# Kernel optimization log

Measured on AMD Instinct MI355X. Metric: run time of the kernel, lower is better.

Reference implementation:

```python
import jax, jax.numpy as jnp
import numpy as np

N = 50000   # nodes
E = 800000  # edges (avg degree 16)
G = 64      # graphs in batch
H = 4       # attention heads
D = 128     # hidden dim per head (= hidden_dim)
V = 128     # embedding vocab (input_dim)
NEG_SLOPE = 0.2

def setup_inputs() -> dict:
    key = jax.random.key(0)
    ks = jax.random.split(key, 12)
    s = 0.05
    return {
        "feats": jax.random.randint(ks[0], (N,), 0, V),
        "src": jax.random.randint(ks[1], (E,), 0, N),
        "dst": jax.random.randint(ks[2], (E,), 0, N),
        "graph_ids": jnp.sort(jax.random.randint(ks[3], (N,), 0, G)),
        "emb": jax.random.normal(ks[4], (V, D)) * s,
        "W1": jax.random.normal(ks[5], (D, H * D)) * s,
        "b1": jax.random.normal(ks[6], (H * D,)) * s,
        "a1": jax.random.normal(ks[7], (H, D)) * s,
        "W2": jax.random.normal(ks[8], (D, H * D)) * s,
        "b2": jax.random.normal(ks[9], (H * D,)) * s,
        "a2": jax.random.normal(ks[10], (H, D)) * s,
        "Wreg": jax.random.normal(ks[11], (1, D)) * s,
    }

def gatv2_layer(x, W, b, a, src, dst):
    # shared-weight GATv2: h = Wx + b, split into heads -> [N,H,D]
    h = (x @ W + b).reshape(-1, H, D)
    hs = h[src]                      # [E,H,D] source feats per edge
    hd = h[dst]                      # [E,H,D] dest feats per edge
    e = jax.nn.leaky_relu(hs + hd, NEG_SLOPE)
    logits = jnp.einsum('ehd,hd->eh', e, a)          # [E,H]
    # edge softmax over incoming edges of each dst node
    m = jax.ops.segment_max(logits, dst, num_segments=N)
    m = jnp.where(jnp.isfinite(m), m, 0.0)           # empty segments -> 0 (unused)
    ex = jnp.exp(logits - m[dst])
    denom = jax.ops.segment_sum(ex, dst, num_segments=N)
    alpha = ex / denom[dst]                          # [E,H]
    rst = jax.ops.segment_sum(alpha[:, :, None] * hs, dst, num_segments=N)  # [N,H,D]
    return rst.mean(axis=1)          # .mean(dim=1) over heads -> [N,D]

def reference(feats, src, dst, graph_ids, emb, W1, b1, a1, W2, b2, a2, Wreg):
    x = emb[feats]                                   # embedding lookup [N,D]
    x = gatv2_layer(x, W1, b1, a1, src, dst)         # layer 1 (dropout=0)
    x = gatv2_layer(x, W2, b2, a2, src, dst)         # layer 2
    pooled = jax.ops.segment_sum(x, graph_ids, num_segments=G)  # SumPooling [G,D]
    return pooled @ Wreg.T                           # Linear bias=False -> [G,1]
```

## Files before the change

kernel.cpp:

```cpp
#include <hip/hip_runtime.h>
#include <hip/hip_bf16.h>

#define N_NODES 50000
#define N_EDGES 800000
#define G_GRAPHS 64
#define H_HEADS 4
#define D_DIM 128
#define HD 512
#define V_VOCAB 128
#define NEG_SLOPE 0.2f

typedef float f32x2v __attribute__((ext_vector_type(2)));
typedef float f32x4 __attribute__((ext_vector_type(4)));
typedef short s16x8 __attribute__((ext_vector_type(8)));
typedef _Float16 h16x2 __attribute__((ext_vector_type(2)));

static __device__ __forceinline__ unsigned short f2b(float f) {
    union { float f; unsigned int i; } x; x.f = f;
    unsigned int r = x.i + 0x7fffu + ((x.i >> 16) & 1u);
    return (unsigned short)(r >> 16);
}
static __device__ __forceinline__ h16x2 u2h2(unsigned int u) {
    union { unsigned int u; h16x2 h; } c; c.u = u; return c.h;
}
static __device__ __forceinline__ unsigned int h22u(h16x2 h) {
    union { unsigned int u; h16x2 h; } c; c.h = h; return c.u;
}
static __device__ __forceinline__ h16x2 packf2(float lo, float hi) {
    union { __fp16 __attribute__((ext_vector_type(2))) p; h16x2 h; } c;
    c.p = __builtin_amdgcn_cvt_pkrtz(lo, hi);
    return c.h;
}

#if __has_builtin(__builtin_amdgcn_cvt_scalef32_pk_f16_fp8)
static __device__ __forceinline__ void fp8x4_to_h16(unsigned int u, h16x2& h0, h16x2& h1) {
    auto r0 = __builtin_amdgcn_cvt_scalef32_pk_f16_fp8((int)u, 1.0f, false);
    auto r1 = __builtin_amdgcn_cvt_scalef32_pk_f16_fp8((int)u, 1.0f, true);
    union { decltype(r0) p; h16x2 h; } c0, c1;
    c0.p = r0; c1.p = r1;
    h0 = c0.h; h1 = c1.h;
}
#else
static __device__ __forceinline__ void fp8x4_to_h16(unsigned int u, h16x2& h0, h16x2& h1) {
    f32x2v lo = __builtin_amdgcn_cvt_pk_f32_fp8(u, false);
    f32x2v hi = __builtin_amdgcn_cvt_pk_f32_fp8(u, true);
    h0 = packf2(lo.x, lo.y);
    h1 = packf2(hi.x, hi.y);
}
#endif

template<int CTRL>
static __device__ __forceinline__ float dpp_add(float v) {
    union { float f; int i; } a, b;
    a.f = v;
    b.i = __builtin_amdgcn_mov_dpp(a.i, CTRL, 0xF, 0xF, true);
    return v + b.f;
}
static __device__ __forceinline__ float row16_sum(float p) {
    p = dpp_add<0xB1>(p);
    p = dpp_add<0x4E>(p);
    p = dpp_add<0x141>(p);
    p = dpp_add<0x140>(p);
    return p;
}

#define MEGA_M1_BLOCKS   64
#define MEGA_WSZ_BLOCKS  256
#define MEGA_HIST_BLOCKS ((N_EDGES + 255) / 256)
__global__ void __launch_bounds__(256) mega_kernel(const float* __restrict__ emb,
                                                   const float* __restrict__ W1,
                                                   const float* __restrict__ b1,
                                                   unsigned int* __restrict__ M1b,
                                                   const float* __restrict__ W2,
                                                   unsigned short* __restrict__ Wb,
                                                   const int* __restrict__ dst,
                                                   int* __restrict__ counts,
                                                   float* __restrict__ pool) {
    int b = blockIdx.x;
    if (b < MEGA_M1_BLOCKS) {
        int idx = b * 256 + threadIdx.x;
        int v = idx >> 7, c0 = (idx & 127) * 4;
        float acc[4] = {b1[c0], b1[c0 + 1], b1[c0 + 2], b1[c0 + 3]};
        for (int k = 0; k < 128; k++) {
            float e = emb[v * 128 + k];
            #pragma unroll
            for (int j = 0; j < 4; j++) acc[j] = fmaf(e, W1[k * 512 + c0 + j], acc[j]);
        }
        unsigned int pk = __builtin_amdgcn_cvt_pk_fp8_f32(acc[0], acc[1], 0, false);
        pk = __builtin_amdgcn_cvt_pk_fp8_f32(acc[2], acc[3], pk, true);
        M1b[idx] = pk;
    } else if (b < MEGA_M1_BLOCKS + MEGA_WSZ_BLOCKS) {
        int idx = (b - MEGA_M1_BLOCKS) * 256 + threadIdx.x;
        int j = idx & 7, c = (idx >> 3) & 511, qq = idx >> 12;
        Wb[idx] = f2b(W2[(qq * 8 + j) * 512 + c]);
    } else {
        int hb = b - MEGA_M1_BLOCKS - MEGA_WSZ_BLOCKS;
        if (hb == 0 && threadIdx.x < G_GRAPHS) pool[threadIdx.x] = 0.f;
        int i = hb * 256 + threadIdx.x;
        if (i < N_EDGES) atomicAdd(&counts[dst[i]], 1);
    }
}

__global__ void __launch_bounds__(256) scanf_kernel(const int* __restrict__ counts,
                                                    int* __restrict__ offsets,
                                                    int* __restrict__ cursor,
                                                    int* __restrict__ bsum,
                                                    int* __restrict__ flag) {
    __shared__ int buf[256];
    __shared__ int sbase;
    int t = threadIdx.x, b = blockIdx.x;
    int i0 = (b * 256 + t) * 4;
    int v[4], c[4], s = 0;
    #pragma unroll
    for (int j = 0; j < 4; j++) {
        int idx = i0 + j;
        v[j] = (idx < N_NODES) ? counts[idx] : 0;
        s += v[j];
        c[j] = s;
    }
    buf[t] = s;
    __syncthreads();
    for (int off = 1; off < 256; off <<= 1) {
        int add = (t >= off) ? buf[t - off] : 0;
        __syncthreads();
        buf[t] += add;
        __syncthreads();
    }
    int ebase = (t > 0) ? buf[t - 1] : 0;
    if (t == 0) {
        bsum[b] = buf[255];
        __threadfence();
        atomicAdd(flag, 1);
        while (atomicAdd(flag, 0) < 64) __builtin_amdgcn_s_sleep(8);
    }
    __syncthreads();
    if (t < 64) {
        int vv = (t < b) ? atomicAdd(&bsum[t], 0) : 0;
        #pragma unroll
        for (int off = 1; off < 64; off <<= 1) vv += __shfl_xor(vv, off);
        if (t == 0) sbase = vv;
    }
    __syncthreads();
    int base = sbase;
    #pragma unroll
    for (int j = 0; j < 4; j++) {
        int idx = i0 + j;
        if (idx < N_NODES) {
            int e = base + ebase + c[j];
            offsets[idx + 1] = e;
            cursor[idx] = e - v[j];
        }
    }
    if (b == 0 && t == 0) offsets[0] = 0;
}

__global__ void scatter_kernel(const int* __restrict__ src, const int* __restrict__ dst,
                               int* __restrict__ cursor, int* __restrict__ csr_src) {
    int i = blockIdx.x * blockDim.x + threadIdx.x;
    if (i < N_EDGES) {
        int d = dst[i];
        int pos = atomicAdd(&cursor[d], 1);
        csr_src[pos] = src[i];
    }
}

template<bool LAYER1>
__global__ void __launch_bounds__(256) gat_kernel(const unsigned int* __restrict__ h,
                                                  const int* __restrict__ offsets,
                                                  const int* __restrict__ csr_src,
                                                  const int* __restrict__ feats,
                                                  const float* __restrict__ a,
                                                  const float* __restrict__ wreg,
                                                  unsigned short* __restrict__ x,
                                                  float* __restrict__ dots) {
    int wid = threadIdx.x >> 6;
    int lane = threadIdx.x & 63;
    int n = blockIdx.x * 4 + wid;
    if (n >= N_NODES) return;
    n = __builtin_amdgcn_readfirstlane(n);
    int row_s = __builtin_amdgcn_readfirstlane(offsets[n]);
    int row_e = __builtin_amdgcn_readfirstlane(offsets[n + 1]);
    int cnt = row_e - row_s;
    int voff = lane * 2;

    h16x2 hd2[4], a06[4], a04[4], acc2[4];
    float pd;
    {
        int nr = LAYER1 ? __builtin_amdgcn_readfirstlane(feats[n]) : n;
        uint2 hv = *reinterpret_cast<const uint2*>(&h[(unsigned)nr * 128u + voff]);
        fp8x4_to_h16(hv.x, hd2[0], hd2[1]);
        fp8x4_to_h16(hv.y, hd2[2], hd2[3]);
        float4 av0 = *reinterpret_cast<const float4*>(&a[lane * 8]);
        float4 av1 = *reinterpret_cast<const float4*>(&a[lane * 8 + 4]);
        float aa[8] = {av0.x, av0.y, av0.z, av0.w, av1.x, av1.y, av1.z, av1.w};
        const float L2E = 1.4426950408889634f;
        #pragma unroll
        for (int k = 0; k < 4; k++) {
            a06[k][0] = (_Float16)(aa[2*k]   * (0.6f * L2E));
            a06[k][1] = (_Float16)(aa[2*k+1] * (0.6f * L2E));
            a04[k][0] = (_Float16)(aa[2*k]   * (0.4f * L2E));
            a04[k][1] = (_Float16)(aa[2*k+1] * (0.4f * L2E));
            acc2[k][0] = (_Float16)0.f; acc2[k][1] = (_Float16)0.f;
        }
        float s = 0.f;
        #pragma unroll
        for (int k = 0; k < 4; k++) s = __builtin_amdgcn_fdot2(hd2[k], a06[k], s, false);
        pd = row16_sum(s);
    }

    auto ld = [&](int ii) {
        int s = __builtin_amdgcn_readfirstlane(csr_src[row_s + ii]);
        if (LAYER1) s = __builtin_amdgcn_readfirstlane(feats[s]);
        return *reinterpret_cast<const uint2*>(&h[(unsigned)s * 128u + voff]);
    };

    float den = 0.f;
    uint2 rA = make_uint2(0, 0), rB = make_uint2(0, 0);
    if (cnt > 0) rA = ld(0);
    if (cnt > 1) rB = ld(1);

    const float C1 = 0.69314718f, C2 = 0.24022651f, C3 = 0.05550411f;

    auto process = [&](uint2 sv) {
        h16x2 hs[4];
        fp8x4_to_h16(sv.x, hs[0], hs[1]);
        fp8x4_to_h16(sv.y, hs[2], hs[3]);
        float p0 = 0.f, p1 = 0.f;
        #pragma unroll
        for (int k = 0; k < 2; k++) {
            h16x2 t2 = hs[k] + hd2[k];
            h16x2 at2 = u2h2(h22u(t2) & 0x7FFF7FFFu);
            p0 = __builtin_amdgcn_fdot2(hs[k], a06[k], p0, false);
            p0 = __builtin_amdgcn_fdot2(at2, a04[k], p0, false);
        }
        #pragma unroll
        for (int k = 2; k < 4; k++) {
            h16x2 t2 = hs[k] + hd2[k];
            h16x2 at2 = u2h2(h22u(t2) & 0x7FFF7FFFu);
            p1 = __builtin_amdgcn_fdot2(hs[k], a06[k], p1, false);
            p1 = __builtin_amdgcn_fdot2(at2, a04[k], p1, false);
        }
        float p = row16_sum(p0 + p1) + pd;
        float w = fmaf(p, fmaf(p, fmaf(p, C3, C2), C1), 1.f);
        den += w;
        h16x2 w2 = packf2(w, w);
        #pragma unroll
        for (int k = 0; k < 4; k++) acc2[k] = w2 * hs[k] + acc2[k];
    };

    for (int i = 0; i < cnt; i += 2) {
        {
            uint2 cur = rA;
            rA = ld(min(i + 2, cnt - 1));
            process(cur);
        }
        if (i + 1 < cnt) {
            uint2 cur = rB;
            rB = ld(min(i + 3, cnt - 1));
            process(cur);
        }
    }

    float inv = (den > 0.f) ? 0.25f / den : 0.f;
    float out8[8];
    #pragma unroll
    for (int j = 0; j < 8; j++) {
        float r = (float)acc2[j >> 1][j & 1] * inv;
        r += __shfl_xor(r, 16);
        r += __shfl_xor(r, 32);
        out8[j] = r;
    }
    if constexpr (LAYER1) {
        if (lane < 16) {
            union { unsigned short u[8]; uint4 v; } o;
            #pragma unroll
            for (int j = 0; j < 8; j++) o.u[j] = f2b(out8[j]);
            *reinterpret_cast<uint4*>(&x[(unsigned)n * 128u + lane * 8]) = o.v;
        }
    } else {
        int d0 = (lane & 15) * 8;
        float4 wv0 = *reinterpret_cast<const float4*>(&wreg[d0]);
        float4 wv1 = *reinterpret_cast<const float4*>(&wreg[d0 + 4]);
        float pdot = out8[0] * wv0.x + out8[1] * wv0.y + out8[2] * wv0.z + out8[3] * wv0.w
                   + out8[4] * wv1.x + out8[5] * wv1.y + out8[6] * wv1.z + out8[7] * wv1.w;
        pdot = row16_sum(pdot);
        if (lane == 0) dots[n] = pdot;
    }
}

__global__ void __launch_bounds__(256) gemm_kernel(const unsigned short* __restrict__ x,
                                                   const unsigned short* __restrict__ Wb,
                                                   const float* __restrict__ bias,
                                                   unsigned char* __restrict__ hout) {
    int w = threadIdx.x >> 6, l = threadIdx.x & 63;
    int rb = blockIdx.y * 64 + w * 16;
    int cb = blockIdx.x * 64;
    int lr = l & 15, lq = l >> 4;
    f32x4 acc[4] = {};
    int arow = rb + lr;
    bool rok = arow < N_NODES;
    #pragma unroll
    for (int s = 0; s < 4; s++) {
        s16x8 afr = {};
        if (rok) afr = *reinterpret_cast<const s16x8*>(&x[(size_t)arow * 128 + s * 32 + lq * 8]);
        #pragma unroll
        for (int sub = 0; sub < 4; sub++) {
            s16x8 bfr = *reinterpret_cast<const s16x8*>(
                &Wb[(((size_t)(s * 4 + lq) * 512) + cb + sub * 16 + lr) << 3]);
            acc[sub] = __builtin_amdgcn_mfma_f32_16x16x32_bf16(bfr, afr, acc[sub], 0, 0, 0);
        }
    }
    if (!rok) return;
    #pragma unroll
    for (int sub = 0; sub < 4; sub++) {
        int col0 = cb + sub * 16 + lq * 4;
        float4 bb = *reinterpret_cast<const float4*>(&bias[col0]);
        unsigned int pk = __builtin_amdgcn_cvt_pk_fp8_f32(acc[sub][0] + bb.x,
                                                          acc[sub][1] + bb.y, 0, false);
        pk = __builtin_amdgcn_cvt_pk_fp8_f32(acc[sub][2] + bb.z,
                                             acc[sub][3] + bb.w, pk, true);
        *reinterpret_cast<unsigned int*>(&hout[(size_t)arow * 512 + col0]) = pk;
    }
}

__global__ void __launch_bounds__(256) pool64_kernel(const float* __restrict__ dots,
                                                     const int* __restrict__ gid,
                                                     float* __restrict__ pool,
                                                     int* __restrict__ done,
                                                     float* __restrict__ out) {
    int wave = (blockIdx.x * blockDim.x + threadIdx.x) >> 6;
    int lane = threadIdx.x & 63;
    int n0 = wave * 64;
    if (n0 < N_NODES) {
        int n = n0 + lane;
        int nc = min(n, N_NODES - 1);
        int g = gid[nc];
        float v = (n < N_NODES) ? dots[n] : 0.f;
        int g0 = __shfl(g, 0);
        bool uni = __all(g == g0);
        if (uni) {
            v += __shfl_xor(v, 1);
            v += __shfl_xor(v, 2);
            v += __shfl_xor(v, 4);
            v += __shfl_xor(v, 8);
            v += __shfl_xor(v, 16);
            v += __shfl_xor(v, 32);
            if (lane == 0) atomicAdd(&pool[g0], v);
        } else {
            if (n < N_NODES) atomicAdd(&pool[g], v);
        }
    }
    __threadfence();
    __syncthreads();
    __shared__ int amlast;
    if (threadIdx.x == 0)
        amlast = (atomicAdd(done, 1) == (int)gridDim.x - 1) ? 1 : 0;
    __syncthreads();
    if (amlast && threadIdx.x < G_GRAPHS) {
        out[threadIdx.x] = atomicAdd(&pool[threadIdx.x], 0.f);
    }
}

extern "C" void kernel_launch(void* const* d_in, const int* in_sizes, int n_in,
                              void* d_out, int out_size, void* d_ws, size_t ws_size,
                              hipStream_t stream) {
    const int* feats = (const int*)d_in[0];
    const int* src   = (const int*)d_in[1];
    const int* dst   = (const int*)d_in[2];
    const int* gids  = (const int*)d_in[3];
    const float* emb  = (const float*)d_in[4];
    const float* W1   = (const float*)d_in[5];
    const float* b1   = (const float*)d_in[6];
    const float* a1   = (const float*)d_in[7];
    const float* W2   = (const float*)d_in[8];
    const float* b2   = (const float*)d_in[9];
    const float* a2   = (const float*)d_in[10];
    const float* wreg = (const float*)d_in[11];
    float* out = (float*)d_out;

    char* ws = (char*)d_ws;
    size_t off = 0;
    auto alloc = [&](size_t bytes) -> void* {
        void* p = ws + off;
        off = (off + bytes + 255) & ~(size_t)255;
        return p;
    };
    int*   counts  = (int*)alloc((size_t)N_NODES * 4 + 8);
    int*   flag    = counts + N_NODES;
    int*   done    = counts + N_NODES + 1;
    int*   offsets = (int*)alloc((size_t)(N_NODES + 1) * 4);
    int*   cursor  = (int*)alloc((size_t)N_NODES * 4);
    int*   csr_src = (int*)alloc((size_t)N_EDGES * 4);
    int*   bsum    = (int*)alloc(64 * 4);
    unsigned int*   M1b = (unsigned int*)alloc((size_t)V_VOCAB * HD);
    unsigned int*   h  = (unsigned int*)alloc((size_t)N_NODES * HD);
    unsigned short* x  = (unsigned short*)alloc((size_t)N_NODES * D_DIM * 2);
    unsigned short* Wb = (unsigned short*)alloc((size_t)D_DIM * HD * 2);
    float* dots    = (float*)alloc((size_t)N_NODES * 4);
    float* pool    = (float*)alloc((size_t)G_GRAPHS * 4);

    hipMemsetAsync(counts, 0, (size_t)N_NODES * 4 + 8, stream);

    mega_kernel<<<MEGA_M1_BLOCKS + MEGA_WSZ_BLOCKS + MEGA_HIST_BLOCKS, 256, 0, stream>>>(
        emb, W1, b1, M1b, W2, Wb, dst, counts, pool);
    scanf_kernel<<<64, 256, 0, stream>>>(counts, offsets, cursor, bsum, flag);
    scatter_kernel<<<(N_EDGES + 255) / 256, 256, 0, stream>>>(src, dst, cursor, csr_src);

    gat_kernel<true><<<(N_NODES + 3) / 4, 256, 0, stream>>>(M1b, offsets, csr_src, feats,
                                                            a1, wreg, x, dots);
    gemm_kernel<<<dim3(8, (N_NODES + 63) / 64), 256, 0, stream>>>(x, Wb, b2, (unsigned char*)h);
    gat_kernel<false><<<(N_NODES + 3) / 4, 256, 0, stream>>>(h, offsets, csr_src, feats,
                                                             a2, wreg, x, dots);

    pool64_kernel<<<(N_NODES / 64 + 4) / 4, 256, 0, stream>>>(dots, gids, pool, done, out);
}
```

Measured before the change: 329.0 us.

## Precompute layer-1 attention weights per vocab pair into a lookup table

Layer-1 node features depend only on the embedding index, so the attention weight for an edge depends only on the (dst feat, src feat) pair. A new kernel precomputes this 128x128x4 table of softmax numerators, and the layer-1 GAT kernel now looks up the weight instead of running per-edge dot products and leaky-relu. This adds a small extra launch and a gathered table read per edge, in exchange for removing per-edge arithmetic in layer 1.

```diff
diff --git a/kernel.cpp b/kernel.cpp
--- a/kernel.cpp
+++ b/kernel.cpp
@@ -101,6 +101,47 @@
     }
 }
 
+__global__ void __launch_bounds__(256) wtab_kernel(const unsigned int* __restrict__ M1b,
+                                                   const float* __restrict__ a,
+                                                   float* __restrict__ Wtab) {
+    int wid = threadIdx.x >> 6, lane = threadIdx.x & 63;
+    int pid = blockIdx.x * 4 + wid;
+    int fd = pid >> 7, fs = pid & 127;
+    int voff = lane * 2;
+
+    h16x2 a06[4], a04[4], hd2[4], hs[4];
+    float4 av0 = *reinterpret_cast<const float4*>(&a[lane * 8]);
+    float4 av1 = *reinterpret_cast<const float4*>(&a[lane * 8 + 4]);
+    float aa[8] = {av0.x, av0.y, av0.z, av0.w, av1.x, av1.y, av1.z, av1.w};
+    const float L2E = 1.4426950408889634f;
+    #pragma unroll
+    for (int k = 0; k < 4; k++) {
+        a06[k][0] = (_Float16)(aa[2*k]   * (0.6f * L2E));
+        a06[k][1] = (_Float16)(aa[2*k+1] * (0.6f * L2E));
+        a04[k][0] = (_Float16)(aa[2*k]   * (0.4f * L2E));
+        a04[k][1] = (_Float16)(aa[2*k+1] * (0.4f * L2E));
+    }
+    uint2 hv = *reinterpret_cast<const uint2*>(&M1b[(unsigned)fd * 128u + voff]);
+    fp8x4_to_h16(hv.x, hd2[0], hd2[1]);
+    fp8x4_to_h16(hv.y, hd2[2], hd2[3]);
+    uint2 sv = *reinterpret_cast<const uint2*>(&M1b[(unsigned)fs * 128u + voff]);
+    fp8x4_to_h16(sv.x, hs[0], hs[1]);
+    fp8x4_to_h16(sv.y, hs[2], hs[3]);
+
+    float p = 0.f;
+    #pragma unroll
+    for (int k = 0; k < 4; k++) {
+        h16x2 t2 = hs[k] + hd2[k];
+        h16x2 at2 = u2h2(h22u(t2) & 0x7FFF7FFFu);
+        p = __builtin_amdgcn_fdot2(t2, a06[k], p, false);
+        p = __builtin_amdgcn_fdot2(at2, a04[k], p, false);
+    }
+    p = row16_sum(p);
+    const float C1 = 0.69314718f, C2 = 0.24022651f, C3 = 0.05550411f;
+    float w = fmaf(p, fmaf(p, fmaf(p, C3, C2), C1), 1.f);
+    if ((lane & 15) == 0) Wtab[pid * 4 + (lane >> 4)] = w;
+}
+
 __global__ void __launch_bounds__(256) scanf_kernel(const int* __restrict__ counts,
                                                     int* __restrict__ offsets,
                                                     int* __restrict__ cursor,
@@ -171,6 +212,7 @@
                                                   const int* __restrict__ feats,
                                                   const float* __restrict__ a,
                                                   const float* __restrict__ wreg,
+                                                  const float* __restrict__ Wtab,
                                                   unsigned short* __restrict__ x,
                                                   float* __restrict__ dots) {
     int wid = threadIdx.x >> 6;
@@ -183,101 +225,136 @@
     int cnt = row_e - row_s;
     int voff = lane * 2;
 
-    h16x2 hd2[4], a06[4], a04[4], acc2[4];
-    float pd;
-    {
-        int nr = LAYER1 ? __builtin_amdgcn_readfirstlane(feats[n]) : n;
-        uint2 hv = *reinterpret_cast<const uint2*>(&h[(unsigned)nr * 128u + voff]);
-        fp8x4_to_h16(hv.x, hd2[0], hd2[1]);
-        fp8x4_to_h16(hv.y, hd2[2], hd2[3]);
-        float4 av0 = *reinterpret_cast<const float4*>(&a[lane * 8]);
-        float4 av1 = *reinterpret_cast<const float4*>(&a[lane * 8 + 4]);
-        float aa[8] = {av0.x, av0.y, av0.z, av0.w, av1.x, av1.y, av1.z, av1.w};
-        const float L2E = 1.4426950408889634f;
+    if constexpr (LAYER1) {
+        int fd = __builtin_amdgcn_readfirstlane(feats[n]);
+        const float* wrow = &Wtab[fd * 512];
+        int woff = lane >> 4;
+        h16x2 acc2[4];
         #pragma unroll
-        for (int k = 0; k < 4; k++) {
-            a06[k][0] = (_Float16)(aa[2*k]   * (0.6f * L2E));
-            a06[k][1] = (_Float16)(aa[2*k+1] * (0.6f * L2E));
-            a04[k][0] = (_Float16)(aa[2*k]   * (0.4f * L2E));
-            a04[k][1] = (_Float16)(aa[2*k+1] * (0.4f * L2E));
-            acc2[k][0] = (_Float16)0.f; acc2[k][1] = (_Float16)0.f;
-        }
-        float s = 0.f;
+        for (int k = 0; k < 4; k++) { acc2[k][0] = (_Float16)0.f; acc2[k][1] = (_Float16)0.f; }
+        float den = 0.f;
+
+        auto ld1 = [&](int ii, uint2& row, float& wv) {
+            int e = __builtin_amdgcn_readfirstlane(csr_src[row_s + ii]);
+            int fs = __builtin_amdgcn_readfirstlane(feats[e]);
+            row = *reinterpret_cast<const uint2*>(&h[(unsigned)fs * 128u + voff]);
+            wv = wrow[fs * 4 + woff];
+        };
+
+        uint2 rA = make_uint2(0, 0), rB = make_uint2(0, 0);
+        float wA = 0.f, wB = 0.f;
+        if (cnt > 0) ld1(0, rA, wA);
+        if (cnt > 1) ld1(1, rB, wB);
+
+        auto proc = [&](uint2 sv, float wv) {
+            h16x2 hs[4];
+            fp8x4_to_h16(sv.x, hs[0], hs[1]);
+            fp8x4_to_h16(sv.y, hs[2], hs[3]);
+            den += wv;
+            h16x2 w2 = packf2(wv, wv);
+            #pragma unroll
+            for (int k = 0; k < 4; k++) acc2[k] = w2 * hs[k] + acc2[k];
+        };
+
+        for (int i = 0; i < cnt; i += 2) {
+            { uint2 c = rA; float wc = wA; ld1(min(i + 2, cnt - 1), rA, wA); proc(c, wc); }
+            if (i + 1 < cnt) { uint2 c = rB; float wc = wB; ld1(min(i + 3, cnt - 1), rB, wB); proc(c, wc); }
+        }
+
+        float inv = (den > 0.f) ? 0.25f / den : 0.f;
+        float out8[8];
         #pragma unroll
-        for (int k = 0; k < 4; k++) s = __builtin_amdgcn_fdot2(hd2[k], a06[k], s, false);
-        pd = row16_sum(s);
-    }
-
-    auto ld = [&](int ii) {
-        int s = __builtin_amdgcn_readfirstlane(csr_src[row_s + ii]);
-        if (LAYER1) s = __builtin_amdgcn_readfirstlane(feats[s]);
-        return *reinterpret_cast<const uint2*>(&h[(unsigned)s * 128u + voff]);
-    };
-
-    float den = 0.f;
-    uint2 rA = make_uint2(0, 0), rB = make_uint2(0, 0);
-    if (cnt > 0) rA = ld(0);
-    if (cnt > 1) rB = ld(1);
-
-    const float C1 = 0.69314718f, C2 = 0.24022651f, C3 = 0.05550411f;
-
-    auto process = [&](uint2 sv) {
-        h16x2 hs[4];
-        fp8x4_to_h16(sv.x, hs[0], hs[1]);
-        fp8x4_to_h16(sv.y, hs[2], hs[3]);
-        float p0 = 0.f, p1 = 0.f;
-        #pragma unroll
-        for (int k = 0; k < 2; k++) {
-            h16x2 t2 = hs[k] + hd2[k];
-            h16x2 at2 = u2h2(h22u(t2) & 0x7FFF7FFFu);
-            p0 = __builtin_amdgcn_fdot2(hs[k], a06[k], p0, false);
-            p0 = __builtin_amdgcn_fdot2(at2, a04[k], p0, false);
-        }
-        #pragma unroll
-        for (int k = 2; k < 4; k++) {
-            h16x2 t2 = hs[k] + hd2[k];
-            h16x2 at2 = u2h2(h22u(t2) & 0x7FFF7FFFu);
-            p1 = __builtin_amdgcn_fdot2(hs[k], a06[k], p1, false);
-            p1 = __builtin_amdgcn_fdot2(at2, a04[k], p1, false);
-        }
-        float p = row16_sum(p0 + p1) + pd;
-        float w = fmaf(p, fmaf(p, fmaf(p, C3, C2), C1), 1.f);
-        den += w;
-        h16x2 w2 = packf2(w, w);
-        #pragma unroll
-        for (int k = 0; k < 4; k++) acc2[k] = w2 * hs[k] + acc2[k];
-    };
-
-    for (int i = 0; i < cnt; i += 2) {
-        {
-            uint2 cur = rA;
-            rA = ld(min(i + 2, cnt - 1));
-            process(cur);
-        }
-        if (i + 1 < cnt) {
-            uint2 cur = rB;
-            rB = ld(min(i + 3, cnt - 1));
-            process(cur);
-        }
-    }
-
-    float inv = (den > 0.f) ? 0.25f / den : 0.f;
-    float out8[8];
-    #pragma unroll
-    for (int j = 0; j < 8; j++) {
-        float r = (float)acc2[j >> 1][j & 1] * inv;
-        r += __shfl_xor(r, 16);
-        r += __shfl_xor(r, 32);
-        out8[j] = r;
-    }
-    if constexpr (LAYER1) {
+        for (int j = 0; j < 8; j++) {
+            float r = (float)acc2[j >> 1][j & 1] * inv;
+            r += __shfl_xor(r, 16);
+            r += __shfl_xor(r, 32);
+            out8[j] = r;
+        }
         if (lane < 16) {
             union { unsigned short u[8]; uint4 v; } o;
             #pragma unroll
             for (int j = 0; j < 8; j++) o.u[j] = f2b(out8[j]);
             *reinterpret_cast<uint4*>(&x[(unsigned)n * 128u + lane * 8]) = o.v;
         }
+        return;
     } else {
+        h16x2 hd2[4], a06[4], a04[4], acc2[4];
+        float pd;
+        {
+            uint2 hv = *reinterpret_cast<const uint2*>(&h[(unsigned)n * 128u + voff]);
+            fp8x4_to_h16(hv.x, hd2[0], hd2[1]);
+            fp8x4_to_h16(hv.y, hd2[2], hd2[3]);
+            float4 av0 = *reinterpret_cast<const float4*>(&a[lane * 8]);
+            float4 av1 = *reinterpret_cast<const float4*>(&a[lane * 8 + 4]);
+            float aa[8] = {av0.x, av0.y, av0.z, av0.w, av1.x, av1.y, av1.z, av1.w};
+            const float L2E = 1.4426950408889634f;
+            #pragma unroll
+            for (int k = 0; k < 4; k++) {
+                a06[k][0] = (_Float16)(aa[2*k]   * (0.6f * L2E));
+                a06[k][1] = (_Float16)(aa[2*k+1] * (0.6f * L2E));
+                a04[k][0] = (_Float16)(aa[2*k]   * (0.4f * L2E));
+                a04[k][1] = (_Float16)(aa[2*k+1] * (0.4f * L2E));
+                acc2[k][0] = (_Float16)0.f; acc2[k][1] = (_Float16)0.f;
+            }
+            float s = 0.f;
+            #pragma unroll
+            for (int k = 0; k < 4; k++) s = __builtin_amdgcn_fdot2(hd2[k], a06[k], s, false);
+            pd = row16_sum(s);
+        }
+
+        auto ld = [&](int ii) {
+            int s = __builtin_amdgcn_readfirstlane(csr_src[row_s + ii]);
+            return *reinterpret_cast<const uint2*>(&h[(unsigned)s * 128u + voff]);
+        };
+
+        float den = 0.f;
+        uint2 rA = make_uint2(0, 0), rB = make_uint2(0, 0);
+        if (cnt > 0) rA = ld(0);
+        if (cnt > 1) rB = ld(1);
+
+        const float C1 = 0.69314718f, C2 = 0.24022651f, C3 = 0.05550411f;
+
+        auto process = [&](uint2 sv) {
+            h16x2 hs[4];
+            fp8x4_to_h16(sv.x, hs[0], hs[1]);
+            fp8x4_to_h16(sv.y, hs[2], hs[3]);
+            float p0 = 0.f, p1 = 0.f;
+            #pragma unroll
+            for (int k = 0; k < 2; k++) {
+                h16x2 t2 = hs[k] + hd2[k];
+                h16x2 at2 = u2h2(h22u(t2) & 0x7FFF7FFFu);
+                p0 = __builtin_amdgcn_fdot2(hs[k], a06[k], p0, false);
+                p0 = __builtin_amdgcn_fdot2(at2, a04[k], p0, false);
+            }
+            #pragma unroll
+            for (int k = 2; k < 4; k++) {
+                h16x2 t2 = hs[k] + hd2[k];
+                h16x2 at2 = u2h2(h22u(t2) & 0x7FFF7FFFu);
+                p1 = __builtin_amdgcn_fdot2(hs[k], a06[k], p1, false);
+                p1 = __builtin_amdgcn_fdot2(at2, a04[k], p1, false);
+            }
+            float p = row16_sum(p0 + p1) + pd;
+            float w = fmaf(p, fmaf(p, fmaf(p, C3, C2), C1), 1.f);
+            den += w;
+            h16x2 w2 = packf2(w, w);
+            #pragma unroll
+            for (int k = 0; k < 4; k++) acc2[k] = w2 * hs[k] + acc2[k];
+        };
+
+        for (int i = 0; i < cnt; i += 2) {
+            { uint2 cur = rA; rA = ld(min(i + 2, cnt - 1)); process(cur); }
+            if (i + 1 < cnt) { uint2 cur = rB; rB = ld(min(i + 3, cnt - 1)); process(cur); }
+        }
+
+        float inv = (den > 0.f) ? 0.25f / den : 0.f;
+        float out8[8];
+        #pragma unroll
+        for (int j = 0; j < 8; j++) {
+            float r = (float)acc2[j >> 1][j & 1] * inv;
+            r += __shfl_xor(r, 16);
+            r += __shfl_xor(r, 32);
+            out8[j] = r;
+        }
         int d0 = (lane & 15) * 8;
         float4 wv0 = *reinterpret_cast<const float4*>(&wreg[d0]);
         float4 wv1 = *reinterpret_cast<const float4*>(&wreg[d0 + 4]);
@@ -396,6 +473,7 @@
     unsigned int*   h  = (unsigned int*)alloc((size_t)N_NODES * HD);
     unsigned short* x  = (unsigned short*)alloc((size_t)N_NODES * D_DIM * 2);
     unsigned short* Wb = (unsigned short*)alloc((size_t)D_DIM * HD * 2);
+    float* Wtab    = (float*)alloc((size_t)V_VOCAB * V_VOCAB * H_HEADS * 4);
     float* dots    = (float*)alloc((size_t)N_NODES * 4);
     float* pool    = (float*)alloc((size_t)G_GRAPHS * 4);
 
@@ -403,14 +481,15 @@
 
     mega_kernel<<<MEGA_M1_BLOCKS + MEGA_WSZ_BLOCKS + MEGA_HIST_BLOCKS, 256, 0, stream>>>(
         emb, W1, b1, M1b, W2, Wb, dst, counts, pool);
+    wtab_kernel<<<(V_VOCAB * V_VOCAB) / 4, 256, 0, stream>>>(M1b, a1, Wtab);
     scanf_kernel<<<64, 256, 0, stream>>>(counts, offsets, cursor, bsum, flag);
     scatter_kernel<<<(N_EDGES + 255) / 256, 256, 0, stream>>>(src, dst, cursor, csr_src);
 
     gat_kernel<true><<<(N_NODES + 3) / 4, 256, 0, stream>>>(M1b, offsets, csr_src, feats,
-                                                            a1, wreg, x, dots);
+                                                            a1, wreg, Wtab, x, dots);
     gemm_kernel<<<dim3(8, (N_NODES + 63) / 64), 256, 0, stream>>>(x, Wb, b2, (unsigned char*)h);
     gat_kernel<false><<<(N_NODES + 3) / 4, 256, 0, stream>>>(h, offsets, csr_src, feats,
-                                                             a2, wreg, x, dots);
+                                                             a2, wreg, Wtab, x, dots);
 
     pool64_kernel<<<(N_NODES / 64 + 4) / 4, 256, 0, stream>>>(dots, gids, pool, done, out);
 }
```

After: 312.3 us. 5.1% less time.
